# Optimization experiments

Hardware: AMD Instinct MI355X
Metric: run time of the kernel (lower is better)

Reference implementation:

```python
import jax, jax.numpy as jnp
import numpy as np

B = 65536          # batch
H_DIM, W_DIM = 8, 8  # feather_size tuple
N = H_DIM * W_DIM    # 64 flat features
INNER = (N + 1) ** 2 # 4225 = outer-product size after prepending ones column
EPS = 1e-6


def setup_inputs() -> dict:
    key = jax.random.key(0)
    k1, k2 = jax.random.split(key, 2)
    x = jax.random.normal(k1, (B, N), jnp.float32)
    # nn.Linear(INNER, N): weight [out, in] = [N, INNER]
    W = jax.random.normal(k2, (N, INNER), jnp.float32) / np.sqrt(INNER)
    b = jnp.zeros((N,), jnp.float32)
    gamma = jnp.ones((N,), jnp.float32)   # LayerNorm scale
    beta = jnp.zeros((N,), jnp.float32)   # LayerNorm shift
    return {"x": x, "W": W, "b": b, "gamma": gamma, "beta": beta}


def reference(x, W, b, gamma, beta):
    Bsz = x.shape[0]
    # prepend ones column: [B, N+1]
    ones = jnp.ones((Bsz, 1), x.dtype)
    x1 = jnp.concatenate([ones, x], axis=-1)
    # bmm outer product x1 @ x1^T per row -> [B, N+1, N+1], flatten to [B, INNER]
    outer = (x1[:, :, None] * x1[:, None, :]).reshape(Bsz, INNER)
    # Linear(INNER -> N)
    y = outer @ W.T + b  # [B, N]
    # UER-py LayerNorm: gamma*(y-u)/sqrt(var+eps)+beta over last dim
    u = jnp.mean(y, axis=-1, keepdims=True)
    s = jnp.mean((y - u) ** 2, axis=-1, keepdims=True)
    y = gamma * (y - u) / jnp.sqrt(s + EPS) + beta
    # final view back to the (out) feather matrix shape
    return y.reshape(Bsz, H_DIM, W_DIM)
```

## Files before the change

### kernel.cpp

```cpp
#include <hip/hip_runtime.h>
#include <stdint.h>
#include <stddef.h>

typedef _Float16 f16;
typedef _Float16 f16x2 __attribute__((ext_vector_type(2)));
typedef _Float16 f16x4 __attribute__((ext_vector_type(4)));
typedef _Float16 f16x8 __attribute__((ext_vector_type(8)));
typedef float f32x16 __attribute__((ext_vector_type(16)));

#define INNER_SZ 4225
#define NQ 164
#define XSTR 72
#define NPH 41

__global__ __launch_bounds__(256) void cm_prep(const float* __restrict__ W,
                                               const float* __restrict__ bias,
                                               f16* __restrict__ Wf2,
                                               float* __restrict__ cvec) {
  int idx = blockIdx.x * 256 + threadIdx.x;
  if (idx < NQ * 1024) {
    int q   = idx >> 10;
    int r10 = idx & 1023;
    int ngh = r10 >> 9;
    int rr  = r10 & 511;
    int G   = rr >> 3;
    int e   = rr & 7;
    int c = G >> 1, hh = G & 1;
    int o = ngh * 32 + c;
    int kl = hh * 8 + e;
    float v = 0.f;
    if (q < 160) {
      int b, start;
      if (q < 16)      { b = 0; start = 0;  }
      else if (q < 48) { b = 1; start = 16; }
      else if (q < 96) { b = 2; start = 48; }
      else             { b = 3; start = 96; }
      int rel = q - start;
      int i = 16 * b + rel / (b + 1);
      int s = rel % (b + 1);
      int j = s * 16 + kl;
      if (j < i)
        v = W[o * INNER_SZ + (i + 1) * 65 + (j + 1)] +
            W[o * INNER_SZ + (j + 1) * 65 + (i + 1)];
      else if (j == i)
        v = W[o * INNER_SZ + (i + 1) * 65 + (i + 1)];
    } else {
      int j = (q - 160) * 16 + kl;
      v = W[o * INNER_SZ + (j + 1)] + W[o * INNER_SZ + (j + 1) * 65];
    }
    Wf2[idx] = (f16)v;
  }
  if (idx < 64) cvec[idx] = W[idx * INNER_SZ] + bias[idx];
}

__device__ inline void gload_lds16(const void* gp, void* lp) {
  __builtin_amdgcn_global_load_lds(
      (const __attribute__((address_space(1))) uint32_t*)(uintptr_t)gp,
      (__attribute__((address_space(3))) uint32_t*)(uintptr_t)lp, 16, 0, 0);
}

__device__ __forceinline__ f16x8 mulsp(f16x2 sp, f16x8 wv) {
  f16x8 r;
#pragma unroll
  for (int e = 0; e < 4; ++e)
    ((f16x2*)&r)[e] = sp * ((const f16x2*)&wv)[e];
  return r;
}

__global__ __launch_bounds__(512, 4) void cm_main(
    const float* __restrict__ x, const f16* __restrict__ Wf2,
    const float* __restrict__ cvec, const float* __restrict__ gamma,
    const float* __restrict__ beta, float* __restrict__ out) {
  __shared__ __align__(16) union SM {
    struct { f16 ring[3][4096]; f16 xs[128 * XSTR]; } k;
    float yt[8192];
  } sm;

  const int tid = threadIdx.x;
  const int lane = tid & 63;
  const int w = tid >> 6;
  const int rowg = w & 3;
  const int ch = w >> 2;
  const int c31 = lane & 31;
  const int h = lane >> 5;
  const long mbase = (long)blockIdx.x * 128;

  const char* wsrc = (const char*)Wf2 + lane * 16;
  char* ringb = (char*)&sm.k.ring[0][0];

#define STAGE(P)                                                            \
  gload_lds16(wsrc + (size_t)(4 * (P) + (w >> 1)) * 2048 + (w & 1) * 1024,  \
              ringb + ((P) % 3) * 8192 + w * 1024)

  STAGE(0);
  STAGE(1);

#pragma unroll
  for (int it = 0; it < 4; ++it) {
    int idx = it * 2048 + tid * 4;
    int row = idx >> 6, col = idx & 63;
    const float4 v = *(const float4*)(x + (size_t)(mbase + row) * 64 + col);
    f16x4 hv = {(f16)v.x, (f16)v.y, (f16)v.z, (f16)v.w};
    *(f16x4*)(sm.k.xs + row * XSTR + col) = hv;
  }
  __syncthreads();

  const int r0 = rowg * 32 + c31;
  f16x8 xw[4];
#pragma unroll
  for (int s = 0; s < 4; ++s)
    xw[s] = *(const f16x8*)(sm.k.xs + r0 * XSTR + s * 16 + h * 8);
#pragma unroll
  for (int s = 0; s < 4; ++s)
    asm volatile("" : "+v"(xw[s]));

  const int bfo = ch * 1024 + (2 * c31 + h) * 16;

  f32x16 acc = (f32x16)(0.0f);
  uint32_t un = *(const uint16_t*)(sm.k.xs + r0 * XSTR);
  f16x2 sp = {};

#pragma unroll
  for (int p = 0; p < NPH; ++p) {
    if (p < NPH - 1) asm volatile("s_waitcnt vmcnt(1)" ::: "memory");
    else             asm volatile("s_waitcnt vmcnt(0)" ::: "memory");
    __builtin_amdgcn_s_barrier();
    asm volatile("" ::: "memory");
    __builtin_amdgcn_sched_barrier(0);
    if (p + 2 < NPH) STAGE(p + 2);
    const char* rb = ringb + (p % 3) * 8192;
    __builtin_amdgcn_s_setprio(1);
#pragma unroll
    for (int kk = 0; kk < 4; ++kk) {
      const int q = 4 * p + kk;
      int i, s, lin;
      if (q >= 160) { i = 64; s = q - 160; lin = 1; }
      else {
        int b = (q < 16) ? 0 : (q < 48) ? 1 : (q < 96) ? 2 : 3;
        int st = (b == 0) ? 0 : (b == 1) ? 16 : (b == 2) ? 48 : 96;
        int rel = q - st;
        i = 16 * b + rel / (b + 1);
        s = rel % (b + 1);
        lin = 0;
      }
      bool newi;
      if (q == 0) newi = true;
      else if (lin) newi = false;
      else {
        int qp = q - 1;
        int bp = (qp < 16) ? 0 : (qp < 48) ? 1 : (qp < 96) ? 2 : 3;
        int stp = (bp == 0) ? 0 : (bp == 1) ? 16 : (bp == 2) ? 48 : 96;
        newi = (16 * bp + (qp - stp) / (bp + 1)) != i;
      }
      if (newi) {
        uint32_t u = un & 0xffffu;
        sp = __builtin_bit_cast(f16x2, u | (u << 16));
        if (i + 1 < 64)
          un = *(const uint16_t*)(sm.k.xs + r0 * XSTR + i + 1);
      }
      f16x8 bf = *(const f16x8*)(rb + kk * 2048 + bfo);
      f16x8 a = lin ? xw[s] : mulsp(sp, xw[s]);
      acc = __builtin_amdgcn_mfma_f32_32x32x16_f16(a, bf, acc, 0, 0, 0);
    }
    __builtin_amdgcn_s_setprio(0);
  }

  __syncthreads();
  {
    const int cg = ch * 32 + c31;
    const int swz = (c31 & 7) << 4;
#pragma unroll
    for (int rq = 0; rq < 4; ++rq) {
      int b0 = cg * 512 + rowg * 128 + rq * 32 + h * 16;
      *(float4*)((char*)sm.yt + (b0 ^ swz)) =
          make_float4(acc[rq * 4 + 0], acc[rq * 4 + 1], acc[rq * 4 + 2], acc[rq * 4 + 3]);
    }
  }
  __syncthreads();

  if (tid < 256) {
    int row = tid >> 1, half = tid & 1;
    float y[32];
    float s = 0.f, qs = 0.f;
#pragma unroll
    for (int j = 0; j < 32; ++j) {
      int c = half * 32 + j;
      int byte = (c * 512 + row * 4) ^ ((c & 7) << 4);
      float v = *(const float*)((const char*)sm.yt + byte);
      v += cvec[c];
      y[j] = v;
      s += v; qs += v * v;
    }
    s  += __shfl_xor(s, 1);
    qs += __shfl_xor(qs, 1);
    float mean = s * 0.015625f;
    float var = qs * 0.015625f - mean * mean;
    float rstd = rsqrtf(var + 1e-6f);
#pragma unroll
    for (int j = 0; j < 32; ++j) {
      int c = half * 32 + j;
      y[j] = gamma[c] * (y[j] - mean) * rstd + beta[c];
    }
    float* op = out + (size_t)(mbase + row) * 64 + half * 32;
#pragma unroll
    for (int j4 = 0; j4 < 8; ++j4)
      *(float4*)(op + j4 * 4) =
          make_float4(y[j4 * 4 + 0], y[j4 * 4 + 1], y[j4 * 4 + 2], y[j4 * 4 + 3]);
  }
#undef STAGE
}

extern "C" void kernel_launch(void* const* d_in, const int* in_sizes, int n_in,
                              void* d_out, int out_size, void* d_ws, size_t ws_size,
                              hipStream_t stream) {
  const float* x     = (const float*)d_in[0];
  const float* W     = (const float*)d_in[1];
  const float* bias  = (const float*)d_in[2];
  const float* gamma = (const float*)d_in[3];
  const float* beta  = (const float*)d_in[4];
  float* out = (float*)d_out;

  f16* Wf2 = (f16*)d_ws;
  float* cvec = (float*)((char*)d_ws + NQ * 1024 * 2);

  cm_prep<<<(NQ * 1024 + 255) / 256, 256, 0, stream>>>(W, bias, Wf2, cvec);
  cm_main<<<512, 512, 0, stream>>>(x, Wf2, cvec, gamma, beta, out);
}
```

Measured before the change: 40.78 us.

## Double K-steps per pipeline phase and split MFMA accumulation into two chains

Each pipeline phase now handles 8 K-slices instead of 4, cutting the phase count from 41 to 21, which halves the number of barriers and waits per block. The ring buffer doubles to hold the larger stages, and the packed weights are padded with zero slices up to 168. Alternating MFMAs between two accumulators breaks the serial dependency chain, and the weight layout is changed to suit a new LDS read offset. The costs are more LDS per block, which may reduce occupancy, and some wasted MFMAs on the zero padding.

```diff
diff --git a/kernel.cpp b/kernel.cpp
--- a/kernel.cpp
+++ b/kernel.cpp
@@ -10,22 +10,24 @@
 
 #define INNER_SZ 4225
 #define NQ 164
+#define NQP 168
+#define KPP 8
+#define NPH 21
 #define XSTR 72
-#define NPH 41
 
 __global__ __launch_bounds__(256) void cm_prep(const float* __restrict__ W,
                                                const float* __restrict__ bias,
                                                f16* __restrict__ Wf2,
                                                float* __restrict__ cvec) {
   int idx = blockIdx.x * 256 + threadIdx.x;
-  if (idx < NQ * 1024) {
+  if (idx < NQP * 1024) {
     int q   = idx >> 10;
     int r10 = idx & 1023;
     int ngh = r10 >> 9;
     int rr  = r10 & 511;
-    int G   = rr >> 3;
+    int hh  = rr >> 8;
+    int c   = (rr >> 3) & 31;
     int e   = rr & 7;
-    int c = G >> 1, hh = G & 1;
     int o = ngh * 32 + c;
     int kl = hh * 8 + e;
     float v = 0.f;
@@ -44,7 +46,7 @@
             W[o * INNER_SZ + (j + 1) * 65 + (i + 1)];
       else if (j == i)
         v = W[o * INNER_SZ + (i + 1) * 65 + (i + 1)];
-    } else {
+    } else if (q < 164) {
       int j = (q - 160) * 16 + kl;
       v = W[o * INNER_SZ + (j + 1)] + W[o * INNER_SZ + (j + 1) * 65];
     }
@@ -72,7 +74,7 @@
     const float* __restrict__ cvec, const float* __restrict__ gamma,
     const float* __restrict__ beta, float* __restrict__ out) {
   __shared__ __align__(16) union SM {
-    struct { f16 ring[3][4096]; f16 xs[128 * XSTR]; } k;
+    struct { f16 ring[3][8192]; f16 xs[128 * XSTR]; } k;
     float yt[8192];
   } sm;
 
@@ -89,8 +91,12 @@
   char* ringb = (char*)&sm.k.ring[0][0];
 
 #define STAGE(P)                                                            \
-  gload_lds16(wsrc + (size_t)(4 * (P) + (w >> 1)) * 2048 + (w & 1) * 1024,  \
-              ringb + ((P) % 3) * 8192 + w * 1024)
+  do {                                                                      \
+    const char* s_ = wsrc + (size_t)(8 * (P) + w) * 2048;                   \
+    char* d_ = ringb + ((P) % 3) * 16384 + w * 2048;                        \
+    gload_lds16(s_, d_);                                                    \
+    gload_lds16(s_ + 1024, d_ + 1024);                                      \
+  } while (0)
 
   STAGE(0);
   STAGE(1);
@@ -114,27 +120,28 @@
   for (int s = 0; s < 4; ++s)
     asm volatile("" : "+v"(xw[s]));
 
-  const int bfo = ch * 1024 + (2 * c31 + h) * 16;
-
-  f32x16 acc = (f32x16)(0.0f);
+  const int bfo = ch * 1024 + c31 * 16 + h * 512;
+
+  f32x16 accA = (f32x16)(0.0f);
+  f32x16 accB = (f32x16)(0.0f);
   uint32_t un = *(const uint16_t*)(sm.k.xs + r0 * XSTR);
   f16x2 sp = {};
 
 #pragma unroll
   for (int p = 0; p < NPH; ++p) {
-    if (p < NPH - 1) asm volatile("s_waitcnt vmcnt(1)" ::: "memory");
+    if (p < NPH - 1) asm volatile("s_waitcnt vmcnt(2)" ::: "memory");
     else             asm volatile("s_waitcnt vmcnt(0)" ::: "memory");
     __builtin_amdgcn_s_barrier();
     asm volatile("" ::: "memory");
     __builtin_amdgcn_sched_barrier(0);
     if (p + 2 < NPH) STAGE(p + 2);
-    const char* rb = ringb + (p % 3) * 8192;
+    const char* rb = ringb + (p % 3) * 16384;
     __builtin_amdgcn_s_setprio(1);
 #pragma unroll
-    for (int kk = 0; kk < 4; ++kk) {
-      const int q = 4 * p + kk;
+    for (int kk = 0; kk < KPP; ++kk) {
+      const int q = 8 * p + kk;
       int i, s, lin;
-      if (q >= 160) { i = 64; s = q - 160; lin = 1; }
+      if (q >= 160) { i = 64; s = (q - 160) & 3; lin = 1; }
       else {
         int b = (q < 16) ? 0 : (q < 48) ? 1 : (q < 96) ? 2 : 3;
         int st = (b == 0) ? 0 : (b == 1) ? 16 : (b == 2) ? 48 : 96;
@@ -160,10 +167,15 @@
       }
       f16x8 bf = *(const f16x8*)(rb + kk * 2048 + bfo);
       f16x8 a = lin ? xw[s] : mulsp(sp, xw[s]);
-      acc = __builtin_amdgcn_mfma_f32_32x32x16_f16(a, bf, acc, 0, 0, 0);
+      if (kk & 1) accB = __builtin_amdgcn_mfma_f32_32x32x16_f16(a, bf, accB, 0, 0, 0);
+      else        accA = __builtin_amdgcn_mfma_f32_32x32x16_f16(a, bf, accA, 0, 0, 0);
     }
     __builtin_amdgcn_s_setprio(0);
   }
+
+  f32x16 acc;
+#pragma unroll
+  for (int r = 0; r < 16; ++r) acc[r] = accA[r] + accB[r];
 
   __syncthreads();
   {
@@ -221,8 +233,8 @@
   float* out = (float*)d_out;
 
   f16* Wf2 = (f16*)d_ws;
-  float* cvec = (float*)((char*)d_ws + NQ * 1024 * 2);
-
-  cm_prep<<<(NQ * 1024 + 255) / 256, 256, 0, stream>>>(W, bias, Wf2, cvec);
+  float* cvec = (float*)((char*)d_ws + NQP * 1024 * 2);
+
+  cm_prep<<<(NQP * 1024 + 255) / 256, 256, 0, stream>>>(W, bias, Wf2, cvec);
   cm_main<<<512, 512, 0, stream>>>(x, Wf2, cvec, gamma, beta, out);
 }
```

New measurement: 39.21 us. 3.9% less time.
